# Performance work log

Hardware: AMD Instinct MI355X
Metric: run time of the kernel (lower is better)

Reference implementation:

```python
import jax, jax.numpy as jnp
import numpy as np

B, N, DIM = 4, 2048, 1024
HEADS, DH = 16, 64
INNER = HEADS * DH
SCALE = 8.0
EPS = 1e-5


def setup_inputs() -> dict:
    key = jax.random.key(0)
    ks = jax.random.split(key, 8)
    x = jax.random.normal(ks[0], (B, N, DIM), dtype=jnp.float32)
    context_mask = jax.random.bernoulli(ks[1], 0.9, (B, N))
    gamma = jnp.ones((DIM,), dtype=jnp.float32)
    null_kv = jax.random.normal(ks[2], (2, HEADS, 1, DH), dtype=jnp.float32)
    Wq = jax.random.normal(ks[3], (DIM, INNER), dtype=jnp.float32) * 0.02
    Wkv = jax.random.normal(ks[4], (DIM, 2 * INNER), dtype=jnp.float32) * 0.02
    # q_scale init: scale / dim_head**-0.5 = 8 * sqrt(64) = 64
    q_scale = jnp.full((DH,), SCALE * (DH ** 0.5), dtype=jnp.float32)
    k_scale = jnp.ones((DH,), dtype=jnp.float32)
    Wout = jax.random.normal(ks[5], (INNER, DIM), dtype=jnp.float32) * 0.02
    return {"x": x, "context_mask": context_mask, "gamma": gamma,
            "null_kv": null_kv, "Wq": Wq, "Wkv": Wkv,
            "q_scale": q_scale, "k_scale": k_scale, "Wout": Wout}


def _l2norm(t):
    return t / jnp.sqrt(jnp.sum(t * t, axis=-1, keepdims=True) + 1e-12)


def reference(x, context_mask, gamma, null_kv, Wq, Wkv, q_scale, k_scale, Wout):
    b, n, _ = x.shape
    # LayerNorm (beta buffer is zeros)
    mu = jnp.mean(x, axis=-1, keepdims=True)
    var = jnp.mean((x - mu) ** 2, axis=-1, keepdims=True)
    xn = (x - mu) / jnp.sqrt(var + EPS) * gamma
    # projections
    q = (xn @ Wq).reshape(b, n, HEADS, DH)
    kv = xn @ Wkv
    k = kv[..., :INNER].reshape(b, n, HEADS, DH)
    v = kv[..., INNER:].reshape(b, n, HEADS, DH)
    # null kv token: [h,1,d] -> [b,1,h,d]
    nk = jnp.broadcast_to(null_kv[0].transpose(1, 0, 2)[None], (b, 1, HEADS, DH))
    nv = jnp.broadcast_to(null_kv[1].transpose(1, 0, 2)[None], (b, 1, HEADS, DH))
    k = jnp.concatenate([nk, k], axis=1)  # [b, n+1, h, d]
    v = jnp.concatenate([nv, v], axis=1)
    # cosine-sim attention with learned per-dim scales
    q = _l2norm(q) * q_scale
    k = _l2norm(k) * k_scale
    # bias from mask (padded True for null token)
    mask = jnp.pad(context_mask, ((0, 0), (1, 0)), constant_values=True)
    bias = jnp.where(mask, 0.0, -10000.0)[:, None, None, :]  # [b,1,1,n+1]
    # memory_efficient_attention applies 1/sqrt(dh) internally
    scores = jnp.einsum('bqhd,bkhd->bhqk', q, k) * (DH ** -0.5) + bias
    attn = jax.nn.softmax(scores, axis=-1)
    out = jnp.einsum('bhqk,bkhd->bqhd', attn, v).reshape(b, n, INNER)
    return out @ Wout
```

## Files before the change

### kernel.cpp

```cpp
#include <hip/hip_runtime.h>
#include <hip/hip_bf16.h>
#include <stdint.h>


using f32x4  = __attribute__((ext_vector_type(4))) float;
using bf16x8 = __attribute__((ext_vector_type(8))) __bf16;
using f16x8  = __attribute__((ext_vector_type(8))) _Float16;
using uintv4 = __attribute__((ext_vector_type(4))) unsigned int;

__device__ __forceinline__ unsigned short f2b(float f) {
    unsigned u = __float_as_uint(f);
    u += 0x7fffu + ((u >> 16) & 1u);
    return (unsigned short)(u >> 16);
}
__device__ __forceinline__ unsigned short f2h(float f) {
    return __builtin_bit_cast(unsigned short, (_Float16)f);
}
__device__ __forceinline__ f32x4 mfma16(bf16x8 a, bf16x8 b, f32x4 c) {
    return __builtin_amdgcn_mfma_f32_16x16x32_bf16(a, b, c, 0, 0, 0);
}
__device__ __forceinline__ f32x4 mfma16h(f16x8 a, f16x8 b, f32x4 c) {
    return __builtin_amdgcn_mfma_f32_16x16x32_f16(a, b, c, 0, 0, 0);
}
__device__ __forceinline__ unsigned pk16(float a, float b) {
    return __builtin_bit_cast(unsigned, __builtin_amdgcn_cvt_pkrtz(a, b));
}
__device__ __forceinline__ void gl_lds16(const void* g, void* l) {
    __builtin_amdgcn_global_load_lds(
        (const __attribute__((address_space(1))) unsigned int*)g,
        (__attribute__((address_space(3))) unsigned int*)l, 16, 0, 0);
}

__global__ __launch_bounds__(256) void transpose_f2b(
    const float* __restrict__ in, unsigned short* __restrict__ out,
    int R, int C)
{
    __shared__ unsigned short t[32][33];
    int tx = threadIdx.x, ty = threadIdx.y;
    int c = blockIdx.x * 32 + tx;
#pragma unroll
    for (int i = 0; i < 4; ++i) {
        int r = blockIdx.y * 32 + ty + i * 8;
        t[ty + i * 8][tx] = f2b(in[(size_t)r * C + c]);
    }
    __syncthreads();
    int r2 = blockIdx.y * 32 + tx;
#pragma unroll
    for (int i = 0; i < 4; ++i) {
        int c2 = blockIdx.x * 32 + ty + i * 8;
        out[(size_t)c2 * R + r2] = t[tx][ty + i * 8];
    }
}

__global__ __launch_bounds__(256) void prep_kernel(
    const float* __restrict__ x, const float* __restrict__ gamma,
    const float* __restrict__ Wq, const float* __restrict__ Wkv,
    const float* __restrict__ null_kv, const float* __restrict__ k_scale,
    unsigned short* __restrict__ xn,
    unsigned short* __restrict__ WqkvT, unsigned short* __restrict__ knull,
    unsigned short* __restrict__ Vt)
{
    __shared__ unsigned short t[32][33];
    __shared__ float ps[4], ps2[4], sh[2];
    const int bid = blockIdx.x;
    const int flat = threadIdx.x + threadIdx.y * 32;

    if (bid < 8192) {
        int row = bid, tid = flat;
        int wave = tid >> 6, lane = tid & 63;
        float4 raw = *(const float4*)(x + ((size_t)row << 10) + (tid << 2));
        float v[4] = { raw.x, raw.y, raw.z, raw.w };
        float s  = v[0] + v[1] + v[2] + v[3];
        float s2 = v[0]*v[0] + v[1]*v[1] + v[2]*v[2] + v[3]*v[3];
#pragma unroll
        for (int off = 1; off < 64; off <<= 1) {
            s  += __shfl_xor(s, off);
            s2 += __shfl_xor(s2, off);
        }
        if (lane == 0) { ps[wave] = s; ps2[wave] = s2; }
        __syncthreads();
        if (tid == 0) {
            float S  = ps[0] + ps[1] + ps[2] + ps[3];
            float S2 = ps2[0] + ps2[1] + ps2[2] + ps2[3];
            float mu  = S * (1.f / 1024.f);
            float var = S2 * (1.f / 1024.f) - mu * mu;
            sh[0] = mu; sh[1] = rsqrtf(var + 1e-5f);
        }
        __syncthreads();
        float mu = sh[0], rstd = sh[1];
        float4 g4 = *(const float4*)(gamma + (tid << 2));
        float g[4] = { g4.x, g4.y, g4.z, g4.w };
        unsigned short o[4];
#pragma unroll
        for (int i = 0; i < 4; ++i) o[i] = f2b((v[i] - mu) * rstd * g[i]);
        uint2 out;
        out.x = (unsigned)o[0] | ((unsigned)o[1] << 16);
        out.y = (unsigned)o[2] | ((unsigned)o[3] << 16);
        *(uint2*)(xn + ((size_t)row << 10) + (tid << 2)) = out;
        return;
    }

    const int bid2 = bid - 8192;
    if (bid2 < 3072) {
        const float* in; unsigned short* out; int C, bx, by;
        if (bid2 < 1024) { in = Wq;  out = WqkvT;              C = 1024;
                           bx = bid2 & 31;  by = bid2 >> 5; }
        else             { int l = bid2 - 1024;
                           in = Wkv; out = WqkvT + (1u << 20); C = 2048;
                           bx = l & 63;     by = l >> 6; }
        int tx = threadIdx.x, ty = threadIdx.y;
        int c = bx * 32 + tx;
#pragma unroll
        for (int i = 0; i < 4; ++i) {
            int r = by * 32 + ty + i * 8;
            t[ty + i * 8][tx] = f2b(in[(size_t)r * C + c]);
        }
        __syncthreads();
        int r2 = by * 32 + tx;
#pragma unroll
        for (int i = 0; i < 4; ++i) {
            int c2 = bx * 32 + ty + i * 8;
            out[(size_t)c2 * 1024 + r2] = t[tx][ty + i * 8];
        }
        return;
    }

    const int nb = bid2 - 3072;
    int wave = flat >> 6, lane = flat & 63;
    int h = nb * 4 + wave;
    int idx = (h << 6) + lane;
    float kvl = null_kv[idx];
    float ss = kvl * kvl;
#pragma unroll
    for (int off = 1; off < 64; off <<= 1) ss += __shfl_xor(ss, off);
    knull[idx] = f2b(kvl * rsqrtf(ss + 1e-12f) * k_scale[lane]);
    unsigned short vn = f2h(null_kv[1024 + idx]);
#pragma unroll
    for (int b = 0; b < 4; ++b)
        Vt[((size_t)(((b << 4) + h) << 6) + lane) * 2056 + 2048] = vn;
    int tt = nb * 256 + flat;
#pragma unroll
    for (int rr = 0; rr < 4; ++rr) {
        size_t row = (size_t)tt * 4 + rr;
#pragma unroll
        for (int c = 0; c < 7; ++c)
            Vt[row * 2056 + 2049 + c] = 0;
    }
}

template<int MODE>
__global__ __launch_bounds__(256, 2) void gemm_bt(
    const unsigned short* __restrict__ A,
    const unsigned short* __restrict__ Bt,
    void* __restrict__ C0,
    unsigned short* __restrict__ Ck,
    unsigned short* __restrict__ Vout,
    const float* __restrict__ qs, const float* __restrict__ ks,
    int K)
{
    __shared__ __align__(16) unsigned char smem[65536];
    __bf16* As = (__bf16*)smem;
    __bf16* Bs = (__bf16*)(smem + 32768);

    int tid = threadIdx.x, lane = tid & 63, wave = tid >> 6;
    int quad = lane >> 4, l15 = lane & 15;
    const int bid = blockIdx.x;
    const int role = bid >> 9;
    const int local = bid & 511;
    const int swztile = ((local & 7) << 6) | (local >> 3);
    int m0 = (swztile >> 3) * 128;
    int n0 = role * 1024 + (swztile & 7) * 128;
    int wm = (wave & 1) * 64, wn = (wave >> 1) * 64;
    f32x4 acc[4][4] = {};

    const int srow8 = lane >> 3;
    const int w7    = lane & 7;
    const int swz   = ((w7 ^ srow8) << 3);
    const unsigned short* gA = A  + (size_t)(m0 + wave * 32 + srow8) * K + swz;
    const unsigned short* gB = Bt + (size_t)(n0 + wave * 32 + srow8) * K + swz;
    const size_t r8 = (size_t)8 * K;

    auto stage = [&](int bf) {
        __bf16* Ab = As + bf * 8192;
        __bf16* Bb = Bs + bf * 8192;
#pragma unroll
        for (int p = 0; p < 4; ++p)
            gl_lds16(gA + p * r8, &Ab[(wave * 32 + p * 8) * 64]);
#pragma unroll
        for (int p = 0; p < 4; ++p)
            gl_lds16(gB + p * r8, &Bb[(wave * 32 + p * 8) * 64]);
        gA += 64; gB += 64;
    };

    stage(0);
    const int nsteps = K >> 6;
    for (int s = 0; s < nsteps; ++s) {
        const int cur = s & 1;
        if (s + 1 < nsteps) {
            stage(cur ^ 1);
            asm volatile("s_waitcnt vmcnt(8)" ::: "memory");
        } else {
            asm volatile("s_waitcnt vmcnt(0)" ::: "memory");
        }
        __builtin_amdgcn_s_barrier();
        __builtin_amdgcn_sched_barrier(0);
        const __bf16* Ab = As + cur * 8192;
        const __bf16* Bb = Bs + cur * 8192;
#pragma unroll
        for (int kk = 0; kk < 2; ++kk) {
            bf16x8 af[4], bfv[4];
#pragma unroll
            for (int i = 0; i < 4; ++i) {
                int row = wm + i * 16 + l15;
                int g = ((kk << 2) + quad) ^ (l15 & 7);
                af[i] = *(const bf16x8*)&Ab[row * 64 + (g << 3)];
            }
#pragma unroll
            for (int j = 0; j < 4; ++j) {
                int row = wn + j * 16 + l15;
                int g = ((kk << 2) + quad) ^ (l15 & 7);
                bfv[j] = *(const bf16x8*)&Bb[row * 64 + (g << 3)];
            }
#pragma unroll
            for (int i = 0; i < 4; ++i)
#pragma unroll
                for (int j = 0; j < 4; ++j)
                    acc[i][j] = mfma16(af[i], bfv[j], acc[i][j]);
        }
        __builtin_amdgcn_sched_barrier(0);
        __builtin_amdgcn_s_barrier();
    }

    if (MODE == 2) {
#pragma unroll
        for (int i = 0; i < 4; ++i)
#pragma unroll
            for (int j = 0; j < 4; ++j) {
                int row = m0 + wm + i * 16 + quad * 4;
                int col = n0 + wn + j * 16 + l15;
                size_t base = (size_t)row * 1024 + col;
#pragma unroll
                for (int r = 0; r < 4; ++r)
                    ((float*)C0)[base + (size_t)r * 1024] = acc[i][j][r];
            }
        return;
    }

    if (n0 >= 2048) {
        unsigned short* tileL = (unsigned short*)smem + wave * 4096;
        int hv = (n0 + wn - 2048) >> 6;
        int bidx = m0 >> 11;
        int tok0w = (m0 + wm) & 2047;
        size_t vbase = (size_t)((((bidx << 4) + hv) << 6)) * 2056;
#pragma unroll
        for (int i = 0; i < 4; ++i)
#pragma unroll
            for (int j = 0; j < 4; ++j) {
                int d = j * 16 + l15;
                int tk = (i * 16 + quad * 4) ^ ((d & 7) << 3);
                unsigned u01 = (unsigned)f2h(acc[i][j][0])
                             | ((unsigned)f2h(acc[i][j][1]) << 16);
                unsigned u23 = (unsigned)f2h(acc[i][j][2])
                             | ((unsigned)f2h(acc[i][j][3]) << 16);
                *(unsigned*)&tileL[d * 64 + tk]     = u01;
                *(unsigned*)&tileL[d * 64 + tk + 2] = u23;
            }
#pragma unroll
        for (int rrr = 0; rrr < 16; ++rrr) {
            int d = rrr * 4 + quad;
            uint2 val = *(const uint2*)
                &tileL[d * 64 + ((l15 * 4) ^ ((d & 7) << 3))];
            *(uint2*)(Vout + vbase + (size_t)d * 2056 + tok0w + l15 * 4) = val;
        }
        return;
    }

    const bool isQ = (n0 < 1024);
    float sc[4];
#pragma unroll
    for (int j = 0; j < 4; ++j) {
        float s = isQ ? qs[j * 16 + l15] : ks[j * 16 + l15];
        sc[j] = isQ ? s * (0.125f * 1.44269504088896f) : s;
    }
    unsigned short* outp = isQ ? (unsigned short*)C0 : Ck;
    const int coln0 = isQ ? n0 : (n0 - 1024);
#pragma unroll
    for (int i = 0; i < 4; ++i)
#pragma unroll
        for (int r = 0; r < 4; ++r) {
            float ss = 0.f;
#pragma unroll
            for (int j = 0; j < 4; ++j) ss += acc[i][j][r] * acc[i][j][r];
            ss += __shfl_xor(ss, 1); ss += __shfl_xor(ss, 2);
            ss += __shfl_xor(ss, 4); ss += __shfl_xor(ss, 8);
            float mul = rsqrtf(ss + 1e-12f);
            size_t rowbase = (size_t)(m0 + wm + i * 16 + quad * 4 + r) * 1024
                           + coln0 + wn + l15;
#pragma unroll
            for (int j = 0; j < 4; ++j) {
                float v = acc[i][j][r];
                outp[rowbase + j * 16] = f2b(v * mul * sc[j]);
            }
        }
}

__global__ __launch_bounds__(256, 4) void attn_kernel(
    const unsigned short* __restrict__ qn,
    const unsigned short* __restrict__ kvK,
    const unsigned short* __restrict__ knull,
    const unsigned short* __restrict__ Vt,
    const int* __restrict__ mask,
    unsigned short* __restrict__ ao)
{
    __shared__ __bf16    Kt[2][64 * 64];
    __shared__ _Float16  Vl[2][64 * 64];
    __shared__ __align__(16) float biasLds[2][64];

    const int tid = threadIdx.x, lane = tid & 63, wave = tid >> 6;
    const int quad = lane >> 4, l15 = lane & 15;
    const int bh = blockIdx.x;
    const int b = bh >> 4, h = bh & 15;
    const int mbase = blockIdx.y * 128 + wave * 32;
    const size_t rowoff = (size_t)b * 2048;

    bf16x8 qf[2][2];
#pragma unroll
    for (int rg = 0; rg < 2; ++rg)
#pragma unroll
        for (int ks = 0; ks < 2; ++ks)
            qf[rg][ks] = *(const bf16x8*)
                &qn[((rowoff + mbase + rg * 16 + l15) << 10) + (h << 6) + ks * 32 + quad * 8];

    const int t8  = lane >> 3;
    const int w7  = lane & 7;
    const int ksc = (w7 ^ t8) << 3;
    const size_t vrow0 = ((size_t)bh << 6);

    const int r0v = wave * 16 + t8;
    const int r1v = wave * 16 + 8 + t8;
    auto Tof = [](int r) {
        return ((r >> 5) << 5) | (((r >> 2) & 3) << 3)
             | (((r >> 4) & 1) << 2) | (r & 3);
    };
    const int T0 = Tof(r0v), T1 = Tof(r1v);

    const unsigned short* kp0 = kvK + ((rowoff + T0) << 10) + (h << 6) + ksc;
    const unsigned short* kp1 = kvK + ((rowoff + T1) << 10) + (h << 6) + ksc;
    const unsigned short* vp0 = Vt + (vrow0 + r0v) * 2056 + ((w7 ^ t8) << 3);
    const unsigned short* vp1 = Vt + (vrow0 + r1v) * 2056 + ((w7 ^ t8) << 3);

    auto issueFast = [&](int bf) {
        gl_lds16(kp0, &Kt[bf][(wave * 16) * 64]);
        gl_lds16(kp1, &Kt[bf][(wave * 16 + 8) * 64]);
        gl_lds16(vp0, &Vl[bf][(wave * 16) * 64]);
        gl_lds16(vp1, &Vl[bf][(wave * 16 + 8) * 64]);
        kp0 += 65536; kp1 += 65536;
        vp0 += 64; vp1 += 64;
    };
    auto issue32 = [&](int bf) {
        const unsigned short* kc =
            kvK + ((rowoff + 2047) << 10) + (h << 6) + ksc;
        const unsigned short* s0 = (T0 == 0) ? knull + (h << 6) + ksc : kc;
        gl_lds16(s0, &Kt[bf][(wave * 16) * 64]);
        gl_lds16(kc, &Kt[bf][(wave * 16 + 8) * 64]);
        gl_lds16(Vt + (vrow0 + r0v) * 2056 + 2048, &Vl[bf][(wave * 16) * 64]);
        gl_lds16(Vt + (vrow0 + r1v) * 2056 + 2048, &Vl[bf][(wave * 16 + 8) * 64]);
    };
    auto biasFor = [&](int nt) -> float {
        int j = (nt << 6) + lane;
        float bv = -512.f;
        if (j < 2048) { if (mask[(b << 11) + j] != 0) bv = 0.f; }
        else if (j == 2048) bv = 0.f;
        return bv;
    };

    const uintv4 onesu = { 0x3c003c00u, 0x3c003c00u, 0x3c003c00u, 0x3c003c00u };
    const f16x8 ones = __builtin_bit_cast(f16x8, onesu);

    f32x4 O[2][4] = {};
    f32x4 rsacc[2] = {};

    issueFast(0);
    float bcur = 0.f;
    if (wave == 0) bcur = biasFor(0);

    for (int nt = 0; nt < 33; ++nt) {
        const int buf = nt & 1;
        if (wave == 0) biasLds[buf][lane] = bcur;
        __syncthreads();
        if (nt < 31) {
            issueFast(buf ^ 1);
            if (wave == 0) bcur = biasFor(nt + 1);
        } else if (nt == 31) {
            issue32(buf ^ 1);
            if (wave == 0) bcur = biasFor(32);
        }

#pragma unroll
        for (int g = 0; g < 2; ++g) {
            float4 b0 = *(const float4*)&biasLds[buf][(g << 5) + (quad << 3)];
            float4 b1 = *(const float4*)&biasLds[buf][(g << 5) + (quad << 3) + 4];
            f32x4 s[2][2];
#pragma unroll
            for (int rg = 0; rg < 2; ++rg) {
                s[rg][0] = f32x4{ b0.x, b0.y, b0.z, b0.w };
                s[rg][1] = f32x4{ b1.x, b1.y, b1.z, b1.w };
            }
#pragma unroll
            for (int t = 0; t < 2; ++t) {
                const __bf16* kb = &Kt[buf][((g * 2 + t) * 16 + l15) * 64];
                bf16x8 k0 = *(const bf16x8*)&kb[(quad ^ (l15 & 7)) << 3];
                bf16x8 k1 = *(const bf16x8*)&kb[((4 + quad) ^ (l15 & 7)) << 3];
#pragma unroll
                for (int rg = 0; rg < 2; ++rg) {
                    s[rg][t] = mfma16(k0, qf[rg][0], s[rg][t]);
                    s[rg][t] = mfma16(k1, qf[rg][1], s[rg][t]);
                }
            }
            f16x8 vf8[4];
#pragma unroll
            for (int dt = 0; dt < 4; ++dt)
                vf8[dt] = *(const f16x8*)
                    &Vl[buf][(dt * 16 + l15) * 64
                             + ((((g << 2) + quad) ^ (l15 & 7)) << 3)];
#pragma unroll
            for (int rg = 0; rg < 2; ++rg) {
                float e0 = __builtin_amdgcn_exp2f(s[rg][0][0]);
                float e1 = __builtin_amdgcn_exp2f(s[rg][0][1]);
                float e2 = __builtin_amdgcn_exp2f(s[rg][0][2]);
                float e3 = __builtin_amdgcn_exp2f(s[rg][0][3]);
                float e4 = __builtin_amdgcn_exp2f(s[rg][1][0]);
                float e5 = __builtin_amdgcn_exp2f(s[rg][1][1]);
                float e6 = __builtin_amdgcn_exp2f(s[rg][1][2]);
                float e7 = __builtin_amdgcn_exp2f(s[rg][1][3]);
                uintv4 pu = { pk16(e0, e1), pk16(e2, e3),
                              pk16(e4, e5), pk16(e6, e7) };
                f16x8 p = __builtin_bit_cast(f16x8, pu);
                rsacc[rg] = mfma16h(p, ones, rsacc[rg]);
#pragma unroll
                for (int dt = 0; dt < 4; ++dt)
                    O[rg][dt] = mfma16h(p, vf8[dt], O[rg][dt]);
            }
        }
    }

#pragma unroll
    for (int rg = 0; rg < 2; ++rg) {
        float inv[4];
#pragma unroll
        for (int r = 0; r < 4; ++r) inv[r] = 1.f / rsacc[rg][r];
#pragma unroll
        for (int dt = 0; dt < 4; ++dt) {
            size_t base = ((rowoff + mbase + rg * 16 + quad * 4) << 10)
                        + (h << 6) + dt * 16 + l15;
#pragma unroll
            for (int r = 0; r < 4; ++r)
                ao[base + ((size_t)r << 10)] = f2b(O[rg][dt][r] * inv[r]);
        }
    }
}

extern "C" void kernel_launch(void* const* d_in, const int* in_sizes, int n_in,
                              void* d_out, int out_size, void* d_ws, size_t ws_size,
                              hipStream_t stream)
{
    const float* x       = (const float*)d_in[0];
    const int*   mask    = (const int*)d_in[1];
    const float* gamma   = (const float*)d_in[2];
    const float* null_kv = (const float*)d_in[3];
    const float* Wq      = (const float*)d_in[4];
    const float* Wkv     = (const float*)d_in[5];
    const float* q_scale = (const float*)d_in[6];
    const float* k_scale = (const float*)d_in[7];
    const float* Wout    = (const float*)d_in[8];

    char* ws = (char*)d_ws;
    const size_t VTG_OFF   = (size_t)48u << 20;
    const size_t VTG_SIZE  = (size_t)4096 * 4112;
    const size_t WQKV_OFF  = VTG_OFF + VTG_SIZE;
    const size_t WQKV_SIZE = (size_t)3072 * 1024 * 2;
    unsigned short* xn    = (unsigned short*)(ws);
    unsigned short* ao    = xn;
    unsigned short* q     = (unsigned short*)(ws + ((size_t)16u << 20));
    unsigned short* WoutT = q;
    unsigned short* kvK   = (unsigned short*)(ws + ((size_t)32u << 20));
    unsigned short* VtG   = (unsigned short*)(ws + VTG_OFF);
    unsigned short* WqkvT = (unsigned short*)(ws + WQKV_OFF);
    unsigned short* knull = (unsigned short*)(ws + WQKV_OFF + WQKV_SIZE);

    prep_kernel<<<dim3(11268), dim3(32, 8), 0, stream>>>(
        x, gamma, Wq, Wkv, null_kv, k_scale, xn, WqkvT, knull, VtG);

    gemm_bt<0><<<dim3(1536), 256, 0, stream>>>(xn, WqkvT, q, kvK, VtG,
                                               q_scale, k_scale, 1024);

    attn_kernel<<<dim3(64, 16), 256, 0, stream>>>(q, kvK, knull, VtG, mask, ao);

    transpose_f2b<<<dim3(32, 32), dim3(32, 8), 0, stream>>>(Wout, WoutT, 1024, 1024);

    gemm_bt<2><<<dim3(512), 256, 0, stream>>>(ao, WoutT, d_out, nullptr, nullptr,
                                              nullptr, nullptr, 1024);
}
```

Measured before the change: 255.3 us.

## Use 256x256 8-wave GEMM for Q/K projections and fold Wout transpose into attention

Moves the Q and K projection parts of the QKV GEMM into a new 512-thread kernel with 256x256 tiles, 128KB dynamic LDS and a phased double-buffered pipeline. The V part stays on the old gemm_bt path via a role offset. The Wout transpose is folded into extra blocks of the attention launch, removing one kernel launch, and WoutT now reuses the WqkvT buffer. The larger tiles aim for more data reuse per block, at the risk of lower occupancy and tricky hand-placed waitcnt/barrier scheduling.

```diff
diff --git a/kernel.cpp b/kernel.cpp
--- a/kernel.cpp
+++ b/kernel.cpp
@@ -29,27 +29,6 @@
     __builtin_amdgcn_global_load_lds(
         (const __attribute__((address_space(1))) unsigned int*)g,
         (__attribute__((address_space(3))) unsigned int*)l, 16, 0, 0);
-}
-
-__global__ __launch_bounds__(256) void transpose_f2b(
-    const float* __restrict__ in, unsigned short* __restrict__ out,
-    int R, int C)
-{
-    __shared__ unsigned short t[32][33];
-    int tx = threadIdx.x, ty = threadIdx.y;
-    int c = blockIdx.x * 32 + tx;
-#pragma unroll
-    for (int i = 0; i < 4; ++i) {
-        int r = blockIdx.y * 32 + ty + i * 8;
-        t[ty + i * 8][tx] = f2b(in[(size_t)r * C + c]);
-    }
-    __syncthreads();
-    int r2 = blockIdx.y * 32 + tx;
-#pragma unroll
-    for (int i = 0; i < 4; ++i) {
-        int c2 = blockIdx.x * 32 + ty + i * 8;
-        out[(size_t)c2 * R + r2] = t[tx][ty + i * 8];
-    }
 }
 
 __global__ __launch_bounds__(256) void prep_kernel(
@@ -148,6 +127,136 @@
     }
 }
 
+__global__ __launch_bounds__(512, 2) void gemm_qk8(
+    const unsigned short* __restrict__ A,
+    const unsigned short* __restrict__ Bt,
+    unsigned short* __restrict__ Cq,
+    unsigned short* __restrict__ Ck,
+    const float* __restrict__ qs, const float* __restrict__ ks)
+{
+    extern __shared__ __bf16 sm8[];
+    __bf16* As = sm8;
+    __bf16* Bs = sm8 + 32768;
+
+    const int tid = threadIdx.x, lane = tid & 63, wave = tid >> 6;
+    const int quad = lane >> 4, l15 = lane & 15;
+    const int bid = blockIdx.x;
+    const int role = bid >> 7;
+    const int local = bid & 127;
+    const int swz = ((local & 7) << 4) | (local >> 3);
+    const int m0 = (swz >> 2) * 256;
+    const int n0 = role * 1024 + (swz & 3) * 256;
+    const int wm = (wave >> 2) * 128;
+    const int wn = (wave & 3) * 64;
+    f32x4 acc[8][4] = {};
+
+    const int r8l = lane >> 3;
+    const int sgr = ((lane & 7) ^ r8l) << 3;
+    const unsigned short* pA = A  + (size_t)(m0 + wave * 16 + r8l) * 1024 + sgr;
+    const unsigned short* pB = Bt + (size_t)(n0 + wave * 16 + r8l) * 1024 + sgr;
+    const int ldsw = (wave * 16) * 64;
+
+    auto stgA = [&](int slot, int half, int kt) {
+        __bf16* d = As + slot * 16384 + half * 8192 + ldsw;
+        const unsigned short* s = pA + (size_t)(half * 128) * 1024 + kt * 64;
+        gl_lds16(s, d);
+        gl_lds16(s + (size_t)8 * 1024, d + 8 * 64);
+    };
+    auto stgB = [&](int slot, int half, int kt) {
+        __bf16* d = Bs + slot * 16384 + half * 8192 + ldsw;
+        const unsigned short* s = pB + (size_t)(half * 128) * 1024 + kt * 64;
+        gl_lds16(s, d);
+        gl_lds16(s + (size_t)8 * 1024, d + 8 * 64);
+    };
+
+    const int ahalf = wm >> 7;
+    const int bhalf = wn >> 7;
+    const int brow  = (wn & 64);
+    bf16x8 bfv[4][2];
+
+    auto phase = [&](int slot, int q, auto stager, bool dovm) {
+        if (q == 0) {
+#pragma unroll
+            for (int j = 0; j < 4; ++j)
+#pragma unroll
+                for (int kk = 0; kk < 2; ++kk)
+                    bfv[j][kk] = *(const bf16x8*)&Bs[slot * 16384 + bhalf * 8192
+                        + (brow + j * 16 + l15) * 64
+                        + ((((kk << 2) + quad) ^ (l15 & 7)) << 3)];
+        }
+        bf16x8 af[2][2];
+#pragma unroll
+        for (int ii = 0; ii < 2; ++ii)
+#pragma unroll
+            for (int kk = 0; kk < 2; ++kk)
+                af[ii][kk] = *(const bf16x8*)&As[slot * 16384 + ahalf * 8192
+                    + ((q * 2 + ii) * 16 + l15) * 64
+                    + ((((kk << 2) + quad) ^ (l15 & 7)) << 3)];
+        stager();
+        if (dovm) asm volatile("s_waitcnt vmcnt(4)" ::: "memory");
+        __builtin_amdgcn_s_barrier();
+        asm volatile("s_waitcnt lgkmcnt(0)" ::: "memory");
+        __builtin_amdgcn_sched_barrier(0);
+#pragma unroll
+        for (int ii = 0; ii < 2; ++ii)
+#pragma unroll
+            for (int kk = 0; kk < 2; ++kk)
+#pragma unroll
+                for (int j = 0; j < 4; ++j)
+                    acc[q * 2 + ii][j] =
+                        mfma16(af[ii][kk], bfv[j][kk], acc[q * 2 + ii][j]);
+        __builtin_amdgcn_sched_barrier(0);
+        __builtin_amdgcn_s_barrier();
+    };
+
+    stgB(0, 0, 0); stgB(0, 1, 0); stgA(0, 0, 0); stgA(0, 1, 0);
+    stgB(1, 0, 1); stgB(1, 1, 1);
+    asm volatile("s_waitcnt vmcnt(4)" ::: "memory");
+    __builtin_amdgcn_s_barrier();
+    __builtin_amdgcn_sched_barrier(0);
+
+    for (int it = 0; it < 8; ++it) {
+        const int k1 = 2 * it + 1;
+        const int k2 = (2 * it + 2) & 15;
+        const int k3 = (2 * it + 3) & 15;
+        phase(0, 0, [&] { stgA(1, 0, k1); }, false);
+        phase(0, 1, [&] { stgA(1, 1, k1); }, false);
+        phase(0, 2, [&] { stgB(0, 0, k2); }, false);
+        phase(0, 3, [&] { stgB(0, 1, k2); }, true);
+        phase(1, 0, [&] { stgA(0, 0, k2); }, false);
+        phase(1, 1, [&] { stgA(0, 1, k2); }, false);
+        phase(1, 2, [&] { stgB(1, 0, k3); }, false);
+        phase(1, 3, [&] { stgB(1, 1, k3); }, true);
+    }
+    asm volatile("s_waitcnt vmcnt(0)" ::: "memory");
+
+    const float* sp = role ? ks : qs;
+    float sc[4];
+#pragma unroll
+    for (int j = 0; j < 4; ++j) {
+        float s = sp[j * 16 + l15];
+        sc[j] = role ? s : s * (0.125f * 1.44269504088896f);
+    }
+    unsigned short* outp = role ? Ck : Cq;
+    const int coln0 = (n0 & 1023) + wn;
+#pragma unroll
+    for (int i = 0; i < 8; ++i)
+#pragma unroll
+        for (int r = 0; r < 4; ++r) {
+            float ss = 0.f;
+#pragma unroll
+            for (int j = 0; j < 4; ++j) ss += acc[i][j][r] * acc[i][j][r];
+            ss += __shfl_xor(ss, 1); ss += __shfl_xor(ss, 2);
+            ss += __shfl_xor(ss, 4); ss += __shfl_xor(ss, 8);
+            float mul = rsqrtf(ss + 1e-12f);
+            size_t rowbase = (size_t)(m0 + wm + i * 16 + quad * 4 + r) * 1024
+                           + coln0 + l15;
+#pragma unroll
+            for (int j = 0; j < 4; ++j)
+                outp[rowbase + j * 16] = f2b(acc[i][j][r] * mul * sc[j]);
+        }
+}
+
 template<int MODE>
 __global__ __launch_bounds__(256, 2) void gemm_bt(
     const unsigned short* __restrict__ A,
@@ -156,7 +265,7 @@
     unsigned short* __restrict__ Ck,
     unsigned short* __restrict__ Vout,
     const float* __restrict__ qs, const float* __restrict__ ks,
-    int K)
+    int roleadd, int K)
 {
     __shared__ __align__(16) unsigned char smem[65536];
     __bf16* As = (__bf16*)smem;
@@ -165,7 +274,7 @@
     int tid = threadIdx.x, lane = tid & 63, wave = tid >> 6;
     int quad = lane >> 4, l15 = lane & 15;
     const int bid = blockIdx.x;
-    const int role = bid >> 9;
+    const int role = (bid >> 9) + roleadd;
     const int local = bid & 511;
     const int swztile = ((local & 7) << 6) | (local >> 3);
     int m0 = (swztile >> 3) * 128;
@@ -297,10 +406,8 @@
             size_t rowbase = (size_t)(m0 + wm + i * 16 + quad * 4 + r) * 1024
                            + coln0 + wn + l15;
 #pragma unroll
-            for (int j = 0; j < 4; ++j) {
-                float v = acc[i][j][r];
-                outp[rowbase + j * 16] = f2b(v * mul * sc[j]);
-            }
+            for (int j = 0; j < 4; ++j)
+                outp[rowbase + j * 16] = f2b(acc[i][j][r] * mul * sc[j]);
         }
 }
 
@@ -310,17 +417,46 @@
     const unsigned short* __restrict__ knull,
     const unsigned short* __restrict__ Vt,
     const int* __restrict__ mask,
-    unsigned short* __restrict__ ao)
+    unsigned short* __restrict__ ao,
+    const float* __restrict__ Wout,
+    unsigned short* __restrict__ WoutT)
 {
     __shared__ __bf16    Kt[2][64 * 64];
     __shared__ _Float16  Vl[2][64 * 64];
     __shared__ __align__(16) float biasLds[2][64];
 
-    const int tid = threadIdx.x, lane = tid & 63, wave = tid >> 6;
+    const int tid = threadIdx.x;
+    if (blockIdx.x >= 1024) {
+        unsigned short (*t32)[33] = (unsigned short (*)[33])Kt;
+        int tb = blockIdx.x - 1024;
+        int tx = tid & 31, ty = tid >> 5;
+#pragma unroll
+        for (int sub = 0; sub < 16; ++sub) {
+            int gx = (tb & 7) * 4 + (sub & 3);
+            int gy = (tb >> 3) * 4 + (sub >> 2);
+            int c = gx * 32 + tx;
+            __syncthreads();
+#pragma unroll
+            for (int i = 0; i < 4; ++i) {
+                int r = gy * 32 + ty + i * 8;
+                t32[ty + i * 8][tx] = f2b(Wout[(size_t)r * 1024 + c]);
+            }
+            __syncthreads();
+            int r2 = gy * 32 + tx;
+#pragma unroll
+            for (int i = 0; i < 4; ++i) {
+                int c2 = gx * 32 + ty + i * 8;
+                WoutT[(size_t)c2 * 1024 + r2] = t32[tx][ty + i * 8];
+            }
+        }
+        return;
+    }
+
+    const int lane = tid & 63, wave = tid >> 6;
     const int quad = lane >> 4, l15 = lane & 15;
-    const int bh = blockIdx.x;
+    const int bh = blockIdx.x & 63;
     const int b = bh >> 4, h = bh & 15;
-    const int mbase = blockIdx.y * 128 + wave * 32;
+    const int mbase = (blockIdx.x >> 6) * 128 + wave * 32;
     const size_t rowoff = (size_t)b * 2048;
 
     bf16x8 qf[2][2];
@@ -482,22 +618,27 @@
     unsigned short* xn    = (unsigned short*)(ws);
     unsigned short* ao    = xn;
     unsigned short* q     = (unsigned short*)(ws + ((size_t)16u << 20));
-    unsigned short* WoutT = q;
     unsigned short* kvK   = (unsigned short*)(ws + ((size_t)32u << 20));
     unsigned short* VtG   = (unsigned short*)(ws + VTG_OFF);
     unsigned short* WqkvT = (unsigned short*)(ws + WQKV_OFF);
+    unsigned short* WoutT = WqkvT;
     unsigned short* knull = (unsigned short*)(ws + WQKV_OFF + WQKV_SIZE);
+
+    hipFuncSetAttribute((const void*)gemm_qk8,
+                        hipFuncAttributeMaxDynamicSharedMemorySize, 131072);
 
     prep_kernel<<<dim3(11268), dim3(32, 8), 0, stream>>>(
         x, gamma, Wq, Wkv, null_kv, k_scale, xn, WqkvT, knull, VtG);
 
-    gemm_bt<0><<<dim3(1536), 256, 0, stream>>>(xn, WqkvT, q, kvK, VtG,
-                                               q_scale, k_scale, 1024);
-
-    attn_kernel<<<dim3(64, 16), 256, 0, stream>>>(q, kvK, knull, VtG, mask, ao);
-
-    transpose_f2b<<<dim3(32, 32), dim3(32, 8), 0, stream>>>(Wout, WoutT, 1024, 1024);
+    gemm_qk8<<<dim3(256), dim3(512), 131072, stream>>>(
+        xn, WqkvT, q, kvK, q_scale, k_scale);
+
+    gemm_bt<0><<<dim3(512), 256, 0, stream>>>(xn, WqkvT, q, kvK, VtG,
+                                              q_scale, k_scale, 2, 1024);
+
+    attn_kernel<<<dim3(1088), 256, 0, stream>>>(q, kvK, knull, VtG, mask, ao,
+                                                Wout, WoutT);
 
     gemm_bt<2><<<dim3(512), 256, 0, stream>>>(ao, WoutT, d_out, nullptr, nullptr,
-                                              nullptr, nullptr, 1024);
-}
+                                              nullptr, nullptr, 0, 1024);
+}
```

After: 252.3 us. No clear change (-1.2%).
